# Optimization experiments

Hardware: AMD Instinct MI355X
Metric: run time of the kernel (lower is better)

The kernel has to match this reference:

```python
import jax, jax.numpy as jnp
import numpy as np

N_NODES = 100000
N_EDGES = 1600000
HIDDEN = 128
N_LAYERS = 4
EPS = 0.0  # GINConv default eps, train_eps=False


def setup_inputs() -> dict:
    key = jax.random.key(0)
    ks = jax.random.split(key, 6)
    scale = 1.0 / np.sqrt(HIDDEN)
    return {
        "x": jax.random.normal(ks[0], (N_NODES, HIDDEN), dtype=jnp.float32),
        "edge_index": jax.random.randint(ks[1], (2, N_EDGES), 0, N_NODES, dtype=jnp.int64),
        "W1": jax.random.normal(ks[2], (N_LAYERS, HIDDEN, HIDDEN), dtype=jnp.float32) * scale,
        "b1": jnp.zeros((N_LAYERS, HIDDEN), dtype=jnp.float32),
        "W2": jax.random.normal(ks[3], (N_LAYERS, HIDDEN, HIDDEN), dtype=jnp.float32) * scale,
        "b2": jnp.zeros((N_LAYERS, HIDDEN), dtype=jnp.float32),
    }


def reference(x, edge_index, W1, b1, W2, b2):
    src = edge_index[0]  # message sources (x_j)
    dst = edge_index[1]  # aggregation targets
    n = x.shape[0]
    for l in range(N_LAYERS):
        x_in = x
        # scatter-add aggregation: sum_{j in N(i)} x_j
        agg = jax.ops.segment_sum(x[src], dst, num_segments=n)
        out = agg + (1.0 + EPS) * x
        # GIN MLP: Linear -> ReLU -> Linear
        h = jax.nn.relu(out @ W1[l] + b1[l]) @ W2[l] + b2[l]
        # outer loop: relu, dropout (identity in eval), residual
        x = x_in + jax.nn.relu(h)
    return x
```

## Files before the change

### kernel.cpp

```cpp
#include <hip/hip_runtime.h>

typedef unsigned short u16;
typedef unsigned int u32;

constexpr int NN = 100000;
constexpr int NE = 1600000;
constexpr int H = 128;

constexpr int NB = 196;
constexpr int BCAP = 10240;
constexpr int PB_E = 4096;
constexpr int PB_BLOCKS = (NE + PB_E - 1) / PB_E;

typedef __bf16 bf16x8 __attribute__((ext_vector_type(8)));
typedef float f32x16 __attribute__((ext_vector_type(16)));

__device__ __forceinline__ u16 f2bf(float f) {
    union { float f; u32 u; } cv; cv.f = f;
    u32 r = (cv.u + 0x7fffu + ((cv.u >> 16) & 1u)) >> 16;
    return (u16)r;
}
__device__ __forceinline__ float bflo(u32 u) {
    union { u32 u; float f; } cv; cv.u = u << 16; return cv.f;
}
__device__ __forceinline__ float bfhi(u32 u) {
    union { u32 u; float f; } cv; cv.u = u & 0xffff0000u; return cv.f;
}

__global__ void detect_kernel(const int* __restrict__ e, int* __restrict__ flag,
                              int* __restrict__ gcursor) {
    __shared__ int anynz;
    if (threadIdx.x == 0) anynz = 0;
    __syncthreads();
    int local = 0;
    for (int i = threadIdx.x; i < 4096; i += 256)
        if (e[2 * i + 1] != 0) local = 1;
    if (local) atomicOr(&anynz, 1);
    __syncthreads();
    if (threadIdx.x == 0) flag[0] = anynz ? 1 : 2;
    if (threadIdx.x < NB) gcursor[threadIdx.x] = 0;
}

__global__ __launch_bounds__(256) void part_kernel(const int* __restrict__ e,
                                                   const int* __restrict__ flag,
                                                   int* __restrict__ gcursor,
                                                   u32* __restrict__ ebuf) {
    __shared__ int lcnt[NB];
    __shared__ int gbaseL[NB];
    const int t = threadIdx.x;
    if (t < NB) lcnt[t] = 0;
    __syncthreads();
    const int st = flag[0];
    const int base = blockIdx.x * PB_E;
    u32 pk[16]; int bk[16]; int rk[16];
#pragma unroll
    for (int j = 0; j < 16; ++j) {
        int i = base + j * 256 + t;
        bk[j] = -1;
        if (i < NE) {
            int s = e[st * i];
            int d = e[st * (NE + i)];
            int b = d >> 9;
            pk[j] = (u32)s | ((u32)(d & 511) << 17);
            bk[j] = b;
            rk[j] = atomicAdd(&lcnt[b], 1);
        }
    }
    __syncthreads();
    if (t < NB) gbaseL[t] = atomicAdd(&gcursor[t], lcnt[t]);
    __syncthreads();
#pragma unroll
    for (int j = 0; j < 16; ++j)
        if (bk[j] >= 0)
            ebuf[bk[j] * BCAP + gbaseL[bk[j]] + rk[j]] = pk[j];
}

__global__ __launch_bounds__(256) void bscan_kernel(const int* __restrict__ gcursor,
                                                    int* __restrict__ bbase,
                                                    int* __restrict__ offs) {
    __shared__ int s[256];
    int t = threadIdx.x;
    int v = (t < NB) ? gcursor[t] : 0;
    s[t] = v;
    __syncthreads();
    for (int off = 1; off < 256; off <<= 1) {
        int u = (t >= off) ? s[t - off] : 0;
        __syncthreads();
        s[t] += u;
        __syncthreads();
    }
    if (t < NB) bbase[t] = s[t] - v;
    if (t == 0) offs[NN] = NE;
}

__global__ __launch_bounds__(256) void bfill_kernel(const u32* __restrict__ ebuf,
                                                    const int* __restrict__ gcursor,
                                                    const int* __restrict__ bbase,
                                                    int* __restrict__ offs,
                                                    int* __restrict__ colv) {
    __shared__ int ncnt[512];
    __shared__ int cur[512];
    __shared__ int ps[256];
    const int b = blockIdx.x, t = threadIdx.x;
    const int En = gcursor[b];
    const int bb = bbase[b];
    ncnt[t] = 0; ncnt[t + 256] = 0;
    __syncthreads();
    const u32* eb = ebuf + b * BCAP;
    for (int i = t; i < En; i += 256)
        atomicAdd(&ncnt[eb[i] >> 17], 1);
    __syncthreads();
    int s2 = ncnt[2 * t] + ncnt[2 * t + 1];
    ps[t] = s2;
    __syncthreads();
    for (int off = 1; off < 256; off <<= 1) {
        int u = (t >= off) ? ps[t - off] : 0;
        __syncthreads();
        ps[t] += u;
        __syncthreads();
    }
    int e0 = ps[t] - s2;
    cur[2 * t] = e0;
    cur[2 * t + 1] = e0 + ncnt[2 * t];
    __syncthreads();
    const int n0 = b * 512;
    for (int i = t; i < 512; i += 256)
        if (n0 + i < NN) offs[n0 + i] = bb + cur[i];
    __syncthreads();
    for (int i = t; i < En; i += 256) {
        u32 p = eb[i];
        int pos = atomicAdd(&cur[p >> 17], 1);
        colv[bb + pos] = (int)(p & 0x1FFFFu);
    }
}

__global__ void wtconv_kernel(const float* __restrict__ W1,
                              const float* __restrict__ W2,
                              u16* __restrict__ wt) {
    int t = blockIdx.x * 256 + threadIdx.x;
    int w = t >> 14;
    int r = t & 16383;
    int k = r >> 7, n = r & 127;
    int l = w >> 1, s = w & 1;
    const float* src = (s == 0 ? W1 : W2) + l * 16384;
    wt[w * 16384 + n * 128 + k] = f2bf(src[k * 128 + n]);
}

__global__ void xinit_kernel(const float* __restrict__ xin,
                             float* __restrict__ x, u16* __restrict__ xb) {
    int i = blockIdx.x * 256 + threadIdx.x;
    float4 v = ((const float4*)xin)[i];
    ((float4*)x)[i] = v;
    uint2 p;
    p.x = (u32)f2bf(v.x) | ((u32)f2bf(v.y) << 16);
    p.y = (u32)f2bf(v.z) | ((u32)f2bf(v.w) << 16);
    ((uint2*)xb)[i] = p;
}

__global__ __launch_bounds__(256) void mlp_kernel(const u16* __restrict__ xbin,
                                                  const int* __restrict__ colv,
                                                  const int* __restrict__ offs,
                                                  const u16* __restrict__ wt1,
                                                  const u16* __restrict__ wt2,
                                                  const float* __restrict__ b1,
                                                  const float* __restrict__ b2,
                                                  float* __restrict__ x,
                                                  u16* __restrict__ xbout) {
    __shared__ u16 lds[32 * 128];
    const int tid = threadIdx.x;
    const int wave = tid >> 6, lane = tid & 63;
    const int ml = lane & 31, g = lane >> 5;
    const int row0 = blockIdx.x * 32;

    {
        const int s0 = wave * 8;
        for (int s = 0; s < 8; ++s) {
            const int r = s0 + s;
            const int node = row0 + r;
            const int rs = __builtin_amdgcn_readfirstlane(offs[node]);
            const int re = __builtin_amdgcn_readfirstlane(offs[node + 1]);
            u32 su = *(const u32*)(xbin + node * H + lane * 2);
            float a0 = bflo(su), a1 = bfhi(su);
            for (int j = rs; j < re; j += 8) {
                int sidx[8];
#pragma unroll
                for (int q = 0; q < 8; ++q) {
                    int idx = j + q;
                    idx = idx < re ? idx : re - 1;
                    sidx[q] = __builtin_amdgcn_readfirstlane(colv[idx]);
                }
                u32 uu[8];
#pragma unroll
                for (int q = 0; q < 8; ++q)
                    uu[q] = *(const u32*)(xbin + sidx[q] * H + lane * 2);
#pragma unroll
                for (int q = 0; q < 8; ++q) {
                    u32 m = (j + q < re) ? 0xffffffffu : 0u;
                    u32 u = uu[q] & m;
                    a0 += bflo(u); a1 += bfhi(u);
                }
            }
            u32 o = (u32)f2bf(a0) | ((u32)f2bf(a1) << 16);
            *(u32*)(&lds[r * H + (((lane >> 2) ^ (r & 15)) << 3) + ((lane & 3) << 1)]) = o;
        }
    }

    bf16x8 bfrag[8];
#pragma unroll
    for (int ks = 0; ks < 8; ++ks)
        bfrag[ks] = *(const bf16x8*)(wt1 + (wave * 32 + ml) * H + ks * 16 + g * 8);

    const float bias1 = b1[wave * 32 + ml];
    const float bias2 = b2[wave * 32 + ml];

    __syncthreads();

    f32x16 acc;
#pragma unroll
    for (int i = 0; i < 16; ++i) acc[i] = 0.f;

#pragma unroll
    for (int ks = 0; ks < 8; ++ks) {
        int chunk = (2 * ks + g) ^ (ml & 15);
        bf16x8 afrag = *(const bf16x8*)(&lds[ml * H + (chunk << 3)]);
        acc = __builtin_amdgcn_mfma_f32_32x32x16_bf16(afrag, bfrag[ks], acc, 0, 0, 0);
    }

    __syncthreads();

#pragma unroll
    for (int reg = 0; reg < 16; ++reg) {
        int rm = (reg & 3) + ((reg >> 2) << 3) + 4 * g;
        int cn = wave * 32 + ml;
        float v = acc[reg] + bias1;
        v = v > 0.f ? v : 0.f;
        lds[rm * H + ((((cn >> 3) ^ (rm & 15))) << 3) + (cn & 7)] = f2bf(v);
    }

#pragma unroll
    for (int ks = 0; ks < 8; ++ks)
        bfrag[ks] = *(const bf16x8*)(wt2 + (wave * 32 + ml) * H + ks * 16 + g * 8);

#pragma unroll
    for (int i = 0; i < 16; ++i) acc[i] = 0.f;

    __syncthreads();

#pragma unroll
    for (int ks = 0; ks < 8; ++ks) {
        int chunk = (2 * ks + g) ^ (ml & 15);
        bf16x8 afrag = *(const bf16x8*)(&lds[ml * H + (chunk << 3)]);
        acc = __builtin_amdgcn_mfma_f32_32x32x16_bf16(afrag, bfrag[ks], acc, 0, 0, 0);
    }

    __syncthreads();

#pragma unroll
    for (int reg = 0; reg < 16; ++reg) {
        int rm = (reg & 3) + ((reg >> 2) << 3) + 4 * g;
        int cn = wave * 32 + ml;
        float v = acc[reg] + bias2;
        v = v > 0.f ? v : 0.f;
        lds[rm * H + ((((cn >> 3) ^ (rm & 15))) << 3) + (cn & 7)] = f2bf(v);
    }

    __syncthreads();

#pragma unroll
    for (int i = 0; i < 2; ++i) {
        int ch = tid + 256 * i;
        int r = ch >> 4, c = ch & 15;
        int gr = row0 + r;
        int4 hv = *(const int4*)(&lds[r * H + ((c ^ (r & 15)) << 3)]);
        float4 x0 = *(const float4*)(x + gr * H + c * 8);
        float4 x1 = *(const float4*)(x + gr * H + c * 8 + 4);
        x0.x += bflo((u32)hv.x); x0.y += bfhi((u32)hv.x);
        x0.z += bflo((u32)hv.y); x0.w += bfhi((u32)hv.y);
        x1.x += bflo((u32)hv.z); x1.y += bfhi((u32)hv.z);
        x1.z += bflo((u32)hv.w); x1.w += bfhi((u32)hv.w);
        *(float4*)(x + gr * H + c * 8) = x0;
        *(float4*)(x + gr * H + c * 8 + 4) = x1;
        int4 xo;
        xo.x = (int)((u32)f2bf(x0.x) | ((u32)f2bf(x0.y) << 16));
        xo.y = (int)((u32)f2bf(x0.z) | ((u32)f2bf(x0.w) << 16));
        xo.z = (int)((u32)f2bf(x1.x) | ((u32)f2bf(x1.y) << 16));
        xo.w = (int)((u32)f2bf(x1.z) | ((u32)f2bf(x1.w) << 16));
        *(int4*)(xbout + gr * H + c * 8) = xo;
    }
}

extern "C" void kernel_launch(void* const* d_in, const int* in_sizes, int n_in,
                              void* d_out, int out_size, void* d_ws, size_t ws_size,
                              hipStream_t stream) {
    const float* x_in = (const float*)d_in[0];
    const int* edges = (const int*)d_in[1];
    const float* W1 = (const float*)d_in[2];
    const float* b1 = (const float*)d_in[3];
    const float* W2 = (const float*)d_in[4];
    const float* b2 = (const float*)d_in[5];
    float* x = (float*)d_out;

    char* ws = (char*)d_ws;
    int* flag = (int*)ws;
    int* gcursor = (int*)(ws + 512);
    int* bbase = (int*)(ws + 2048);
    int* offs = (int*)(ws + 4096);
    int* colv = (int*)(ws + 406528);
    u16* wt = (u16*)(ws + 6809600);
    u16* xb0 = (u16*)(ws + 7072768);
    u16* xb1 = (u16*)(ws + 32672768);
    u32* ebuf = (u32*)xb1;

    detect_kernel<<<1, 256, 0, stream>>>(edges, flag, gcursor);
    part_kernel<<<PB_BLOCKS, 256, 0, stream>>>(edges, flag, gcursor, ebuf);
    bscan_kernel<<<1, 256, 0, stream>>>(gcursor, bbase, offs);
    bfill_kernel<<<NB, 256, 0, stream>>>(ebuf, gcursor, bbase, offs, colv);
    wtconv_kernel<<<131072 / 256, 256, 0, stream>>>(W1, W2, wt);
    xinit_kernel<<<(NN * H / 4) / 256, 256, 0, stream>>>(x_in, x, xb0);

    for (int l = 0; l < 4; ++l) {
        u16* xin = (l & 1) ? xb1 : xb0;
        u16* xout = (l & 1) ? xb0 : xb1;
        mlp_kernel<<<NN / 32, 256, 0, stream>>>(
            xin, colv, offs,
            wt + (l * 2) * 16384, wt + (l * 2 + 1) * 16384,
            b1 + l * 128, b2 + l * 128, x, xout);
    }
}
```

Baseline: 524.2 us.

## Flatten per-wave edge gather across rows with prefetched 16-wide index batches

Each wave now walks the concatenated edge range of its 8 destination rows as one stream, in batches of 16. The next batch of column indices is prefetched while the current gathers are in flight. The row-local id is packed into the high bits of each CSR column entry, so row boundaries are found inline and partial sums are flushed into LDS. The self term is preloaded into LDS with vectorized copies. This removes per-node loop overhead and masked tail waste and raises memory-level parallelism, at the cost of more registers and an extra bf16 rounding when the self term is added.

```diff
diff --git a/kernel.cpp b/kernel.cpp
--- a/kernel.cpp
+++ b/kernel.cpp
@@ -130,7 +130,7 @@
     for (int i = t; i < En; i += 256) {
         u32 p = eb[i];
         int pos = atomicAdd(&cur[p >> 17], 1);
-        colv[bb + pos] = (int)(p & 0x1FFFFu);
+        colv[bb + pos] = (int)((p & 0x1FFFFu) | (((p >> 17) & 31u) << 27));
     }
 }
 
@@ -172,37 +172,62 @@
     const int ml = lane & 31, g = lane >> 5;
     const int row0 = blockIdx.x * 32;
 
+#pragma unroll
+    for (int i = 0; i < 2; ++i) {
+        int ch = tid + 256 * i;
+        int r = ch >> 4, c = ch & 15;
+        int gr = row0 + r;
+        int4 v = *(const int4*)(xbin + gr * H + c * 8);
+        *(int4*)(&lds[r * H + ((c ^ (r & 15)) << 3)]) = v;
+    }
+    __syncthreads();
+
     {
-        const int s0 = wave * 8;
-        for (int s = 0; s < 8; ++s) {
-            const int r = s0 + s;
-            const int node = row0 + r;
-            const int rs = __builtin_amdgcn_readfirstlane(offs[node]);
-            const int re = __builtin_amdgcn_readfirstlane(offs[node + 1]);
-            u32 su = *(const u32*)(xbin + node * H + lane * 2);
-            float a0 = bflo(su), a1 = bfhi(su);
-            for (int j = rs; j < re; j += 8) {
-                int sidx[8];
-#pragma unroll
-                for (int q = 0; q < 8; ++q) {
-                    int idx = j + q;
-                    idx = idx < re ? idx : re - 1;
-                    sidx[q] = __builtin_amdgcn_readfirstlane(colv[idx]);
+        const int node0 = row0 + wave * 8;
+        const int jb = __builtin_amdgcn_readfirstlane(offs[node0]);
+        const int je = __builtin_amdgcn_readfirstlane(offs[node0 + 8]);
+        int cur = wave * 8;
+        float a0 = 0.f, a1 = 0.f;
+        if (jb < je) {
+            u32 ce[16];
+#pragma unroll
+            for (int q = 0; q < 16; ++q) {
+                int idx = jb + q;
+                idx = idx < je ? idx : je - 1;
+                ce[q] = (u32)__builtin_amdgcn_readfirstlane(colv[idx]);
+            }
+            for (int j = jb; j < je; j += 16) {
+                u32 uu[16];
+#pragma unroll
+                for (int q = 0; q < 16; ++q)
+                    uu[q] = *(const u32*)(xbin + (ce[q] & 0x1FFFFu) * H + lane * 2);
+                u32 cn[16];
+#pragma unroll
+                for (int q = 0; q < 16; ++q) {
+                    int idx = j + 16 + q;
+                    idx = idx < je ? idx : je - 1;
+                    cn[q] = (u32)__builtin_amdgcn_readfirstlane(colv[idx]);
                 }
-                u32 uu[8];
-#pragma unroll
-                for (int q = 0; q < 8; ++q)
-                    uu[q] = *(const u32*)(xbin + sidx[q] * H + lane * 2);
-#pragma unroll
-                for (int q = 0; q < 8; ++q) {
-                    u32 m = (j + q < re) ? 0xffffffffu : 0u;
-                    u32 u = uu[q] & m;
-                    a0 += bflo(u); a1 += bfhi(u);
+#pragma unroll
+                for (int q = 0; q < 16; ++q) {
+                    if (j + q < je) {
+                        int rloc = (int)(ce[q] >> 27);
+                        if (rloc != cur) {
+                            u16* p = &lds[cur * H + (((lane >> 2) ^ (cur & 15)) << 3) + ((lane & 3) << 1)];
+                            u32 old = *(u32*)p;
+                            *(u32*)p = (u32)f2bf(bflo(old) + a0) | ((u32)f2bf(bfhi(old) + a1) << 16);
+                            a0 = 0.f; a1 = 0.f; cur = rloc;
+                        }
+                        a0 += bflo(uu[q]); a1 += bfhi(uu[q]);
+                    }
                 }
+#pragma unroll
+                for (int q = 0; q < 16; ++q) ce[q] = cn[q];
             }
-            u32 o = (u32)f2bf(a0) | ((u32)f2bf(a1) << 16);
-            *(u32*)(&lds[r * H + (((lane >> 2) ^ (r & 15)) << 3) + ((lane & 3) << 1)]) = o;
         }
+        u16* p = &lds[cur * H + (((lane >> 2) ^ (cur & 15)) << 3) + ((lane & 3) << 1)];
+        u32 old = *(u32*)p;
+        *(u32*)p = (u32)f2bf(bflo(old) + a0) | ((u32)f2bf(bfhi(old) + a1) << 16);
     }
 
     bf16x8 bfrag[8];
```

Measured after the change: 490.1 us. -6.5%, faster.
